# Optimization experiments

Measured on AMD Instinct MI355X. Metric: run time of the kernel, lower is better.

## Reference

```python
import jax, jax.numpy as jnp
import numpy as np

K_ATTRS = 16  # fixed number of attribute clusters (torch.unique made static for jit)
NEG_INF = jnp.float32(-1e9)


def setup_inputs() -> dict:
    key = jax.random.key(0)
    ks = jax.random.split(key, 20)
    B, T, V, D, H = 4096, 200, 100000, 64, 64
    M0, M1 = 256, 128
    FC_IN = D + D + H + D  # 256
    s = 0.02
    f32 = jnp.float32
    inp = {
        "item_id": jax.random.randint(ks[0], (B,), 0, V),
        "hist_item_ids": jax.random.randint(ks[1], (B, T), 0, V),
        "hist_item_attributes": jax.random.randint(ks[2], (B, T), 0, K_ATTRS),
        "emb_table": s * jax.random.normal(ks[3], (V, D), dtype=f32),
        "au_W1": s * jax.random.normal(ks[4], (4 * D, H), dtype=f32),
        "au_b1": jnp.zeros((H,), f32),
        "au_W2": s * jax.random.normal(ks[5], (H, 1), dtype=f32),
        "au_b2": jnp.zeros((1,), f32),
        "gru_Wx": s * jax.random.normal(ks[6], (D, 3 * H), dtype=f32),
        "gru_Wh": s * jax.random.normal(ks[7], (H, 3 * H), dtype=f32),
        "gru_b": jnp.zeros((3 * H,), f32),
        "fc_W0": s * jax.random.normal(ks[8], (FC_IN, M0), dtype=f32),
        "fc_b0": jnp.zeros((M0,), f32),
        "fc_W1": s * jax.random.normal(ks[9], (M0, M1), dtype=f32),
        "fc_b1": jnp.zeros((M1,), f32),
        "final_W": s * jax.random.normal(ks[10], (M1, 1), dtype=f32),
        "final_b": jnp.zeros((1,), f32),
    }
    return inp


def reference(item_id, hist_item_ids, hist_item_attributes, emb_table,
              au_W1, au_b1, au_W2, au_b2, gru_Wx, gru_Wh, gru_b,
              fc_W0, fc_b0, fc_W1, fc_b1, final_W, final_b):
    item = emb_table[item_id]            # [B,D]
    hist = emb_table[hist_item_ids]      # [B,T,D]
    B = item.shape[0]
    H = gru_Wh.shape[0]

    # --- DIEN: GRU over history, final hidden state ---
    xp = hist @ gru_Wx + gru_b           # [B,T,3H]

    def step(h, x):
        gz, gr, gn = jnp.split(h @ gru_Wh, 3, axis=-1)
        xz, xr, xn = jnp.split(x, 3, axis=-1)
        z = jax.nn.sigmoid(xz + gz)
        r = jax.nn.sigmoid(xr + gr)
        n = jnp.tanh(xn + r * gn)
        return (1.0 - z) * n + z * h, None

    h0 = jnp.zeros((B, H), hist.dtype)
    interest_evolution, _ = jax.lax.scan(step, h0, jnp.swapaxes(xp, 0, 1))  # [B,H]

    # --- DIN-style activation unit: score each key against the target item ---
    def act_unit(q, keys):  # q:[B,D], keys:[B,N,D] -> [B,N,1]
        qe = jnp.broadcast_to(q[:, None, :], keys.shape)
        feat = jnp.concatenate([keys, qe, keys - qe, keys * qe], axis=-1)
        hid = jax.nn.relu(feat @ au_W1 + au_b1)
        return hid @ au_W2 + au_b2

    w1 = act_unit(item, hist)                    # [B,T,1]
    user_interest_l1 = jnp.sum(w1 * hist, axis=1)  # [B,D]

    # --- attribute_group: per-attribute masked softmax + weighted sum ---
    mask = hist_item_attributes[..., None] == jnp.arange(K_ATTRS)  # [B,T,K]
    logits = jnp.where(mask, w1, NEG_INF)        # [B,T,K]
    probs = jax.nn.softmax(logits, axis=1) * mask
    cluster = jnp.einsum('btk,btd->bkd', probs, hist)  # [B,K,D]

    w2 = act_unit(item, cluster)                 # [B,K,1]
    user_interest_l2 = jnp.sum(w2 * cluster, axis=1)  # [B,D]

    combined = jnp.concatenate(
        [user_interest_l1, user_interest_l2, interest_evolution, item], axis=1)
    x = jax.nn.relu(combined @ fc_W0 + fc_b0)
    x = jax.nn.relu(x @ fc_W1 + fc_b1)
    out = x @ final_W + final_b                  # [B,1]
    return jax.nn.sigmoid(out[:, 0])             # [B]
```

## Files before the change

kernel.cpp:

```cpp
#include <hip/hip_runtime.h>
#include <hip/hip_bf16.h>

#define B_   4096
#define T_   200
#define KA   16

#define OFF_BG  0
#define OFF_QP  (OFF_BG  + B_*T_)
#define OFF_UI1 (OFF_QP  + B_*64)
#define OFF_UI2 (OFF_UI1 + B_*64)
#define OFF_HF  (OFF_UI2 + B_*64)
#define OFF_CL  (OFF_HF  + B_*64)

typedef __attribute__((ext_vector_type(8))) short bf16x8;
typedef __attribute__((ext_vector_type(4))) float f32x4;

__device__ __forceinline__ float sigmoidf_(float x) {
  return 1.f / (1.f + __expf(-x));
}
__device__ __forceinline__ float sigf(float x) {
  return __builtin_amdgcn_rcpf(1.f + __builtin_amdgcn_exp2f(-1.44269504f * x));
}
__device__ __forceinline__ float tanhfast(float y) {
  return 1.f - 2.f * __builtin_amdgcn_rcpf(1.f + __builtin_amdgcn_exp2f(2.88539008f * y));
}
__device__ __forceinline__ short f2bf(float x) {
  unsigned u = __float_as_uint(x);
  unsigned r = (u + 0x7fffu + ((u >> 16) & 1u)) >> 16;
  return (short)r;
}
__device__ __forceinline__ unsigned cvtpk(float lo, float hi) {
  unsigned r;
  asm("v_cvt_pk_bf16_f32 %0, %1, %2" : "=v"(r) : "v"(lo), "v"(hi));
  return r;
}
union BF8 { bf16x8 v; unsigned u[4]; };

__device__ __forceinline__ bf16x8 pack8(float4 f0, float4 f1) {
  BF8 a;
  a.u[0] = cvtpk(f0.x, f0.y);
  a.u[1] = cvtpk(f0.z, f0.w);
  a.u[2] = cvtpk(f1.x, f1.y);
  a.u[3] = cvtpk(f1.z, f1.w);
  return a.v;
}
__device__ __forceinline__ bf16x8 pack8m(float4 f0, float4 f1,
                                         float4 q0, float4 q1) {
  BF8 a;
  a.u[0] = cvtpk(f0.x*q0.x, f0.y*q0.y);
  a.u[1] = cvtpk(f0.z*q0.z, f0.w*q0.w);
  a.u[2] = cvtpk(f1.x*q1.x, f1.y*q1.y);
  a.u[3] = cvtpk(f1.z*q1.z, f1.w*q1.w);
  return a.v;
}


__global__ __launch_bounds__(256) void k_act1(
    const int* __restrict__ item_id, const int* __restrict__ hist_ids,
    const int* __restrict__ attrs,
    const float* __restrict__ emb, const float* __restrict__ auW1,
    const float* __restrict__ aub1, const float* __restrict__ auW2,
    const float* __restrict__ aub2,
    float* __restrict__ qp_out, float* __restrict__ ui1_out,
    float* __restrict__ cluster_out, short* __restrict__ bg_out)
{
  __shared__ short sB2[8192];
  __shared__ float sAcc[4][KA][64];
  __shared__ float sW1[208];
  __shared__ float sP[200];
  __shared__ float sM[KA], sE[KA];
  __shared__ float sItem[64], sQp[64];
  __shared__ float sQpP[4][64];
  __shared__ float sUi[4][64];
  __shared__ int   sIds[200], sAttr[200];

  const int b = blockIdx.x;
  const int tid = threadIdx.x;
  const int wave = tid >> 6, lane = tid & 63;
  const int g = lane >> 4;
  const int c15 = lane & 15;
  const int itrow = item_id[b];

  for (int idx = tid; idx < 8192; idx += 256) {
    const int k = idx >> 6, col = idx & 63;
    float v;
    if (k < 64) v = auW1[k*64 + col] + auW1[2*4096 + k*64 + col];
    else        v = auW1[3*4096 + (k-64)*64 + col];
    short bv = f2bf(v);
    int dst = ((k >> 5)*4 + ((k >> 3) & 3))*512 + col*8 + (k & 7);
    sB2[dst] = bv;
    if (b == 0) bg_out[dst] = bv;
  }
  if (tid < 64) sItem[tid] = emb[(size_t)itrow*64 + tid];
  if (tid < T_) {
    sIds[tid]  = hist_ids[(size_t)b*T_ + tid];
    sAttr[tid] = attrs[(size_t)b*T_ + tid];
  }
  for (int i = tid; i < 4*KA*64; i += 256) ((float*)sAcc)[i] = 0.f;
  __syncthreads();

  {
    const int j = tid & 63, iq = tid >> 6;
    float acc = 0.f;
    #pragma unroll
    for (int ii = 0; ii < 16; ++ii) {
      const int i = iq*16 + ii;
      acc += sItem[i] * (auW1[(64+i)*64 + j] - auW1[(128+i)*64 + j]);
    }
    sQpP[iq][j] = acc;
  }
  __syncthreads();
  if (tid < 64) {
    float q = aub1[tid] + sQpP[0][tid] + sQpP[1][tid] + sQpP[2][tid] + sQpP[3][tid];
    sQp[tid] = q;
    qp_out[(size_t)b*64 + tid] = q;
  }
  __syncthreads();

  const float4* itemp = (const float4*)(emb + (size_t)itrow*64);
  float4 q0 = itemp[g*2],     q1 = itemp[g*2 + 1];
  float4 q2 = itemp[8 + g*2], q3 = itemp[8 + g*2 + 1];

  bf16x8 bfr[4][4];
  #pragma unroll
  for (int kk = 0; kk < 4; ++kk) {
    #pragma unroll
    for (int n = 0; n < 4; ++n)
      bfr[kk][n] = *(const bf16x8*)&sB2[(kk*4 + g)*512 + (n*16 + c15)*8];
  }
  float w2v[4], qpv[4];
  #pragma unroll
  for (int n = 0; n < 4; ++n) {
    w2v[n] = auW2[n*16 + c15];
    qpv[n] = sQp[n*16 + c15];
  }
  const float b2v = aub2[0];

  for (int tt = wave; tt < 13; tt += 4) {
    const int t = tt*16 + c15;
    float4 k0{0,0,0,0}, k1{0,0,0,0}, k2{0,0,0,0}, k3{0,0,0,0};
    if (t < T_) {
      const float4* kp = (const float4*)(emb + (size_t)sIds[t]*64);
      k0 = kp[g*2];     k1 = kp[g*2 + 1];
      k2 = kp[8 + g*2]; k3 = kp[8 + g*2 + 1];
    }
    bf16x8 a0 = pack8(k0, k1);
    bf16x8 a1 = pack8(k2, k3);
    bf16x8 a2 = pack8m(k0, k1, q0, q1);
    bf16x8 a3 = pack8m(k2, k3, q2, q3);

    f32x4 acc[4];
    #pragma unroll
    for (int n = 0; n < 4; ++n) acc[n] = f32x4{qpv[n], qpv[n], qpv[n], qpv[n]};
    #pragma unroll
    for (int n = 0; n < 4; ++n) {
      acc[n] = __builtin_amdgcn_mfma_f32_16x16x32_bf16(a0, bfr[0][n], acc[n], 0, 0, 0);
      acc[n] = __builtin_amdgcn_mfma_f32_16x16x32_bf16(a1, bfr[1][n], acc[n], 0, 0, 0);
      acc[n] = __builtin_amdgcn_mfma_f32_16x16x32_bf16(a2, bfr[2][n], acc[n], 0, 0, 0);
      acc[n] = __builtin_amdgcn_mfma_f32_16x16x32_bf16(a3, bfr[3][n], acc[n], 0, 0, 0);
    }
    float ws[4] = {0.f, 0.f, 0.f, 0.f};
    #pragma unroll
    for (int n = 0; n < 4; ++n) {
      #pragma unroll
      for (int r = 0; r < 4; ++r)
        ws[r] += fmaxf(acc[n][r], 0.f) * w2v[n];
    }
    #pragma unroll
    for (int r = 0; r < 4; ++r) {
      ws[r] += __shfl_xor(ws[r], 1);
      ws[r] += __shfl_xor(ws[r], 2);
      ws[r] += __shfl_xor(ws[r], 4);
      ws[r] += __shfl_xor(ws[r], 8);
      ws[r] += b2v;
    }
    if (c15 == 0) {
      #pragma unroll
      for (int r = 0; r < 4; ++r) {
        const int trow = tt*16 + g*4 + r;
        if (trow < T_) sW1[trow] = ws[r];
      }
    }
  }
  __syncthreads();

  for (int k = wave; k < KA; k += 4) {
    float m = -1e9f;
    for (int tt4 = 0; tt4 < 4; ++tt4) {
      int t = tt4*64 + lane;
      if (t < T_ && sAttr[t] == k) m = fmaxf(m, sW1[t]);
    }
    #pragma unroll
    for (int off = 32; off > 0; off >>= 1) m = fmaxf(m, __shfl_xor(m, off));
    float e = 0.f;
    for (int tt4 = 0; tt4 < 4; ++tt4) {
      int t = tt4*64 + lane;
      if (t < T_ && sAttr[t] == k) e += __expf(sW1[t] - m);
    }
    #pragma unroll
    for (int off = 32; off > 0; off >>= 1) e += __shfl_xor(e, off);
    if (lane == 0) { sM[k] = m; sE[k] = e; }
  }
  __syncthreads();
  if (tid < T_) {
    int k = sAttr[tid];
    float e = sE[k];
    sP[tid] = (e > 0.f) ? __expf(sW1[tid] - sM[k]) * __builtin_amdgcn_rcpf(e) : 0.f;
  }
  __syncthreads();

  float uiacc = 0.f;
  for (int t = wave; t < T_; t += 4) {
    int k    = sAttr[t];
    float p  = sP[t];
    float wv = sW1[t];
    float v  = emb[(size_t)sIds[t]*64 + lane];
    sAcc[wave][k][lane] += p * v;
    uiacc += wv * v;
  }
  sUi[wave][lane] = uiacc;
  __syncthreads();

  for (int i = tid; i < KA*64; i += 256) {
    cluster_out[(size_t)b*(KA*64) + i] =
        sAcc[0][0][i] + sAcc[1][0][i] + sAcc[2][0][i] + sAcc[3][0][i];
  }
  if (tid < 64) {
    ui1_out[(size_t)b*64 + tid] =
        sUi[0][tid] + sUi[1][tid] + sUi[2][tid] + sUi[3][tid];
  }
}

#define GRU_ROWS 16
__global__ __launch_bounds__(512) void k_gru(
    const int* __restrict__ hist_ids, const float* __restrict__ emb,
    const float* __restrict__ Wx, const float* __restrict__ Wh,
    const float* __restrict__ gb, float* __restrict__ hfin_out)
{
  __shared__ short sH[2][16*64];
  __shared__ short sX[4][16*64];
  __shared__ int   sIds[16*200];

  const int tid  = threadIdx.x;
  const int w    = tid >> 6;
  const int lane = tid & 63;
  const int g    = lane >> 4;
  const int c15  = lane & 15;
  const int b0   = blockIdx.x * GRU_ROWS;

  for (int i = tid; i < 16*200; i += 512) {
    const int r = i / 200, t = i - r*200;
    sIds[i] = hist_ids[(size_t)(b0 + r)*T_ + t];
  }
  for (int i = tid; i < 16*64; i += 512) sH[0][i] = 0;
  __syncthreads();

  if (w >= 4) {
    const int stane = (w - 4)*64 + lane;
    const int srow  = stane >> 4;
    const int scol  = (stane & 15) * 4;
    const int sidx  = srow*64 + (((scol >> 3) ^ (srow & 7))*8) + (scol & 7);
    const int* idrow = &sIds[srow*200];
    #pragma unroll
    for (int p = 0; p < 2; ++p) {
      const float4 f = *(const float4*)(emb + (size_t)idrow[p]*64 + scol);
      uint2 u; u.x = cvtpk(f.x, f.y); u.y = cvtpk(f.z, f.w);
      *(uint2*)&sX[p][sidx] = u;
    }
    __syncthreads();
    for (int t = 0; t < T_; ++t) {
      const int t2 = (t + 2 < T_) ? (t + 2) : (T_ - 1);
      const float4 f = *(const float4*)(emb + (size_t)idrow[t2]*64 + scol);
      uint2 u; u.x = cvtpk(f.x, f.y); u.y = cvtpk(f.z, f.w);
      *(uint2*)&sX[(t + 2) & 3][sidx] = u;
      __syncthreads();
    }
  } else {
    bf16x8 bx[3][2], bh[3][2];
    #pragma unroll
    for (int l = 0; l < 3; ++l) {
      const int jb = (l*4 + w)*16 + c15;
      #pragma unroll
      for (int kk = 0; kk < 2; ++kk) {
        bf16x8 vx, vh;
        #pragma unroll
        for (int e = 0; e < 8; ++e) {
          const int krow = kk*32 + g*8 + e;
          vx[e] = f2bf(Wx[(size_t)krow*192 + jb]);
          vh[e] = f2bf(Wh[(size_t)krow*192 + jb]);
        }
        bx[l][kk] = vx; bh[l][kk] = vh;
      }
    }
    float bias[3];
    #pragma unroll
    for (int l = 0; l < 3; ++l) bias[l] = gb[l*64 + w*16 + c15];

    const int rs = c15 & 7;
    const int ridx0 = c15*64 + ((g    ) ^ rs)*8;
    const int ridx1 = c15*64 + ((g + 4) ^ rs)*8;
    int widx[4];
    {
      const int unit = w*2 + (c15 >> 3);
      #pragma unroll
      for (int r = 0; r < 4; ++r) {
        const int row = g*4 + r;
        widx[r] = row*64 + ((unit ^ (row & 7))*8) + (c15 & 7);
      }
    }
    float hold[4] = {0.f, 0.f, 0.f, 0.f};
    __syncthreads();

    #pragma unroll 2
    for (int t = 0; t < T_; ++t) {
      const short* hbuf = sH[t & 1];
      short*       hnxt = sH[(t & 1) ^ 1];
      const short* xbuf = sX[t & 3];

      bf16x8 ax0 = *(const bf16x8*)&xbuf[ridx0];
      bf16x8 ax1 = *(const bf16x8*)&xbuf[ridx1];
      bf16x8 ah0 = *(const bf16x8*)&hbuf[ridx0];
      bf16x8 ah1 = *(const bf16x8*)&hbuf[ridx1];

      f32x4 aX[3], aH[3];
      #pragma unroll
      for (int l = 0; l < 3; ++l) {
        aX[l] = f32x4{bias[l], bias[l], bias[l], bias[l]};
        aH[l] = f32x4{0.f, 0.f, 0.f, 0.f};
      }
      #pragma unroll
      for (int l = 0; l < 3; ++l) {
        aH[l] = __builtin_amdgcn_mfma_f32_16x16x32_bf16(ah0, bh[l][0], aH[l], 0, 0, 0);
        aH[l] = __builtin_amdgcn_mfma_f32_16x16x32_bf16(ah1, bh[l][1], aH[l], 0, 0, 0);
        aX[l] = __builtin_amdgcn_mfma_f32_16x16x32_bf16(ax0, bx[l][0], aX[l], 0, 0, 0);
        aX[l] = __builtin_amdgcn_mfma_f32_16x16x32_bf16(ax1, bx[l][1], aX[l], 0, 0, 0);
      }

      #pragma unroll
      for (int r = 0; r < 4; ++r) {
        float z  = sigf(aX[0][r] + aH[0][r]);
        float rr = sigf(aX[1][r] + aH[1][r]);
        float nn = tanhfast(aX[2][r] + rr * aH[2][r]);
        hold[r] = nn + z * (hold[r] - nn);
        hnxt[widx[r]] = f2bf(hold[r]);
      }
      __syncthreads();
    }

    #pragma unroll
    for (int r = 0; r < 4; ++r)
      hfin_out[(size_t)(b0 + g*4 + r)*64 + w*16 + c15] = hold[r];
  }
}

__global__ __launch_bounds__(256) void k_act2(
    const int* __restrict__ item_id, const float* __restrict__ emb,
    const float* __restrict__ auW2, const float* __restrict__ aub2,
    const float* __restrict__ qp_in, const float* __restrict__ cluster_in,
    const short* __restrict__ bg_in, float* __restrict__ ui2_out)
{
  __shared__ short sB2[8192];
  __shared__ float sWs[4][16];
  __shared__ float sWf[16];
  __shared__ float sUi[4][64];

  const int b = blockIdx.x;
  const int tid = threadIdx.x;
  const int wave = tid >> 6, lane = tid & 63;
  const int g = lane >> 4;
  const int c15 = lane & 15;
  const int itrow = item_id[b];

  for (int i = tid; i < 4096; i += 256)
    ((unsigned*)sB2)[i] = ((const unsigned*)bg_in)[i];
  __syncthreads();

  const float4* itemp = (const float4*)(emb + (size_t)itrow*64);
  float4 q0 = itemp[g*2],     q1 = itemp[g*2 + 1];
  float4 q2 = itemp[8 + g*2], q3 = itemp[8 + g*2 + 1];
  const float4* kp = (const float4*)(cluster_in + (size_t)b*(KA*64) + c15*64);
  float4 k0 = kp[g*2],     k1 = kp[g*2 + 1];
  float4 k2 = kp[8 + g*2], k3 = kp[8 + g*2 + 1];
  bf16x8 a0 = pack8(k0, k1);
  bf16x8 a1 = pack8(k2, k3);
  bf16x8 a2 = pack8m(k0, k1, q0, q1);
  bf16x8 a3 = pack8m(k2, k3, q2, q3);

  const float qpv = qp_in[(size_t)b*64 + wave*16 + c15];
  const float w2v = auW2[wave*16 + c15];
  f32x4 acc = f32x4{qpv, qpv, qpv, qpv};
  acc = __builtin_amdgcn_mfma_f32_16x16x32_bf16(a0, *(const bf16x8*)&sB2[(0*4+g)*512 + (wave*16+c15)*8], acc, 0, 0, 0);
  acc = __builtin_amdgcn_mfma_f32_16x16x32_bf16(a1, *(const bf16x8*)&sB2[(1*4+g)*512 + (wave*16+c15)*8], acc, 0, 0, 0);
  acc = __builtin_amdgcn_mfma_f32_16x16x32_bf16(a2, *(const bf16x8*)&sB2[(2*4+g)*512 + (wave*16+c15)*8], acc, 0, 0, 0);
  acc = __builtin_amdgcn_mfma_f32_16x16x32_bf16(a3, *(const bf16x8*)&sB2[(3*4+g)*512 + (wave*16+c15)*8], acc, 0, 0, 0);

  float ws[4];
  #pragma unroll
  for (int r = 0; r < 4; ++r) {
    float v = fmaxf(acc[r], 0.f) * w2v;
    v += __shfl_xor(v, 1);
    v += __shfl_xor(v, 2);
    v += __shfl_xor(v, 4);
    v += __shfl_xor(v, 8);
    ws[r] = v;
  }
  if (c15 == 0) {
    #pragma unroll
    for (int r = 0; r < 4; ++r) sWs[wave][g*4 + r] = ws[r];
  }
  __syncthreads();
  if (tid < KA)
    sWf[tid] = sWs[0][tid] + sWs[1][tid] + sWs[2][tid] + sWs[3][tid] + aub2[0];
  __syncthreads();

  float uiacc = 0.f;
  #pragma unroll
  for (int kk = 0; kk < 4; ++kk) {
    const int k = wave*4 + kk;
    uiacc += sWf[k] * cluster_in[(size_t)b*(KA*64) + k*64 + lane];
  }
  sUi[wave][lane] = uiacc;
  __syncthreads();
  if (tid < 64) {
    ui2_out[(size_t)b*64 + tid] =
        sUi[0][tid] + sUi[1][tid] + sUi[2][tid] + sUi[3][tid];
  }
}

#define MLP_ROWS 16
__global__ __launch_bounds__(256) void k_mlp(
    const int* __restrict__ item_id, const float* __restrict__ emb,
    const float* __restrict__ ui1, const float* __restrict__ ui2,
    const float* __restrict__ hfin,
    const float* __restrict__ W0, const float* __restrict__ b0,
    const float* __restrict__ W1, const float* __restrict__ b1,
    const float* __restrict__ fW, const float* __restrict__ fb,
    float* __restrict__ out)
{
  __shared__ float sC[MLP_ROWS][256];
  __shared__ float sX0[MLP_ROWS][256];
  __shared__ float sX1[MLP_ROWS][128];
  const int tid = threadIdx.x;
  const int rb  = blockIdx.x * MLP_ROWS;

  for (int idx = tid; idx < MLP_ROWS*256; idx += 256) {
    int r = idx >> 8, c = idx & 255;
    size_t row = (size_t)(rb + r);
    float v;
    if (c < 64)       v = ui1[row*64 + c];
    else if (c < 128) v = ui2[row*64 + (c-64)];
    else if (c < 192) v = hfin[row*64 + (c-128)];
    else              v = emb[(size_t)item_id[row]*64 + (c-192)];
    sC[r][c] = v;
  }
  __syncthreads();
  {
    float acc[MLP_ROWS];
    #pragma unroll
    for (int r = 0; r < MLP_ROWS; ++r) acc[r] = b0[tid];
    #pragma unroll 4
    for (int i = 0; i < 256; ++i) {
      float w = W0[(size_t)i*256 + tid];
      #pragma unroll
      for (int r = 0; r < MLP_ROWS; ++r) acc[r] += sC[r][i] * w;
    }
    #pragma unroll
    for (int r = 0; r < MLP_ROWS; ++r) sX0[r][tid] = fmaxf(acc[r], 0.f);
  }
  __syncthreads();
  if (tid < 128) {
    float acc[MLP_ROWS];
    #pragma unroll
    for (int r = 0; r < MLP_ROWS; ++r) acc[r] = b1[tid];
    #pragma unroll 4
    for (int i = 0; i < 256; ++i) {
      float w = W1[(size_t)i*128 + tid];
      #pragma unroll
      for (int r = 0; r < MLP_ROWS; ++r) acc[r] += sX0[r][i] * w;
    }
    #pragma unroll
    for (int r = 0; r < MLP_ROWS; ++r) sX1[r][tid] = fmaxf(acc[r], 0.f);
  }
  __syncthreads();
  {
    int r = tid >> 4, l16 = tid & 15;
    float p = 0.f;
    for (int i = l16; i < 128; i += 16) p += sX1[r][i] * fW[i];
    #pragma unroll
    for (int off = 8; off > 0; off >>= 1) p += __shfl_xor(p, off);
    if (l16 == 0) {
      float logit = p + fb[0];
      out[rb + r] = sigmoidf_(logit);
    }
  }
}

extern "C" void kernel_launch(void* const* d_in, const int* in_sizes, int n_in,
                              void* d_out, int out_size, void* d_ws, size_t ws_size,
                              hipStream_t stream)
{
  const int*   item_id  = (const int*)d_in[0];
  const int*   hist_ids = (const int*)d_in[1];
  const int*   attrs    = (const int*)d_in[2];
  const float* emb      = (const float*)d_in[3];
  const float* auW1     = (const float*)d_in[4];
  const float* aub1     = (const float*)d_in[5];
  const float* auW2     = (const float*)d_in[6];
  const float* aub2     = (const float*)d_in[7];
  const float* gWx      = (const float*)d_in[8];
  const float* gWh      = (const float*)d_in[9];
  const float* gb       = (const float*)d_in[10];
  const float* W0       = (const float*)d_in[11];
  const float* b0       = (const float*)d_in[12];
  const float* W1       = (const float*)d_in[13];
  const float* b1       = (const float*)d_in[14];
  const float* fW       = (const float*)d_in[15];
  const float* fb       = (const float*)d_in[16];

  float* out = (float*)d_out;
  float* ws  = (float*)d_ws;
  short* bg      = (short*)(ws + OFF_BG);
  float* qp      = ws + OFF_QP;
  float* ui1     = ws + OFF_UI1;
  float* ui2     = ws + OFF_UI2;
  float* hfin    = ws + OFF_HF;
  float* cluster = ws + OFF_CL;

  k_act1<<<B_, 256, 0, stream>>>(item_id, hist_ids, attrs, emb, auW1, aub1,
                                 auW2, aub2, qp, ui1, cluster, bg);
  k_gru<<<B_/GRU_ROWS, 512, 0, stream>>>(hist_ids, emb, gWx, gWh, gb, hfin);
  k_act2<<<B_, 256, 0, stream>>>(item_id, emb, auW2, aub2, qp, cluster, bg,
                                 ui2);
  k_mlp<<<B_/MLP_ROWS, 256, 0, stream>>>(item_id, emb, ui1, ui2, hfin,
                                         W0, b0, W1, b1, fW, fb, out);
}
```

Before: 361.6 us.

## Precompute bf16 activation-unit weights once in a prep kernel, alias LDS, prefetch gathers

```diff
diff --git a/kernel.cpp b/kernel.cpp
--- a/kernel.cpp
+++ b/kernel.cpp
@@ -6,6 +6,7 @@
 #define KA   16
 
 #define OFF_BG  0
+#define OFF_WQ  4096
 #define OFF_QP  (OFF_BG  + B_*T_)
 #define OFF_UI1 (OFF_QP  + B_*64)
 #define OFF_UI2 (OFF_UI1 + B_*64)
@@ -55,17 +56,34 @@
 }
 
 
+__global__ __launch_bounds__(256) void k_prep(
+    const float* __restrict__ auW1, short* __restrict__ bg,
+    float* __restrict__ wq)
+{
+  const int i = blockIdx.x*256 + threadIdx.x;
+  if (i < 8192) {
+    const int k = i >> 6, col = i & 63;
+    float v;
+    if (k < 64) v = auW1[k*64 + col] + auW1[2*4096 + k*64 + col];
+    else        v = auW1[3*4096 + (k-64)*64 + col];
+    bg[((k >> 5)*4 + ((k >> 3) & 3))*512 + col*8 + (k & 7)] = f2bf(v);
+  } else if (i < 12288) {
+    const int j = i - 8192;
+    wq[j] = auW1[(64 + (j >> 6))*64 + (j & 63)]
+          - auW1[(128 + (j >> 6))*64 + (j & 63)];
+  }
+}
+
 __global__ __launch_bounds__(256) void k_act1(
     const int* __restrict__ item_id, const int* __restrict__ hist_ids,
     const int* __restrict__ attrs,
-    const float* __restrict__ emb, const float* __restrict__ auW1,
-    const float* __restrict__ aub1, const float* __restrict__ auW2,
-    const float* __restrict__ aub2,
+    const float* __restrict__ emb, const float* __restrict__ aub1,
+    const float* __restrict__ auW2, const float* __restrict__ aub2,
+    const short* __restrict__ bg_in, const float* __restrict__ wq_in,
     float* __restrict__ qp_out, float* __restrict__ ui1_out,
-    float* __restrict__ cluster_out, short* __restrict__ bg_out)
+    float* __restrict__ cluster_out)
 {
-  __shared__ short sB2[8192];
-  __shared__ float sAcc[4][KA][64];
+  __shared__ __align__(16) char sPool[16384];
   __shared__ float sW1[208];
   __shared__ float sP[200];
   __shared__ float sM[KA], sE[KA];
@@ -74,6 +92,9 @@
   __shared__ float sUi[4][64];
   __shared__ int   sIds[200], sAttr[200];
 
+  short* sB2 = (short*)sPool;
+  float (*sAcc)[KA][64] = (float (*)[KA][64])sPool;
+
   const int b = blockIdx.x;
   const int tid = threadIdx.x;
   const int wave = tid >> 6, lane = tid & 63;
@@ -81,22 +102,13 @@
   const int c15 = lane & 15;
   const int itrow = item_id[b];
 
-  for (int idx = tid; idx < 8192; idx += 256) {
-    const int k = idx >> 6, col = idx & 63;
-    float v;
-    if (k < 64) v = auW1[k*64 + col] + auW1[2*4096 + k*64 + col];
-    else        v = auW1[3*4096 + (k-64)*64 + col];
-    short bv = f2bf(v);
-    int dst = ((k >> 5)*4 + ((k >> 3) & 3))*512 + col*8 + (k & 7);
-    sB2[dst] = bv;
-    if (b == 0) bg_out[dst] = bv;
-  }
+  for (int i = tid; i < 4096; i += 256)
+    ((unsigned*)sB2)[i] = ((const unsigned*)bg_in)[i];
   if (tid < 64) sItem[tid] = emb[(size_t)itrow*64 + tid];
   if (tid < T_) {
     sIds[tid]  = hist_ids[(size_t)b*T_ + tid];
     sAttr[tid] = attrs[(size_t)b*T_ + tid];
   }
-  for (int i = tid; i < 4*KA*64; i += 256) ((float*)sAcc)[i] = 0.f;
   __syncthreads();
 
   {
@@ -105,7 +117,7 @@
     #pragma unroll
     for (int ii = 0; ii < 16; ++ii) {
       const int i = iq*16 + ii;
-      acc += sItem[i] * (auW1[(64+i)*64 + j] - auW1[(128+i)*64 + j]);
+      acc += sItem[i] * wq_in[i*64 + j];
     }
     sQpP[iq][j] = acc;
   }
@@ -135,6 +147,9 @@
     qpv[n] = sQp[n*16 + c15];
   }
   const float b2v = aub2[0];
+  __syncthreads();
+
+  for (int i = tid; i < 4*KA*64; i += 256) ((float*)sAcc)[i] = 0.f;
 
   for (int tt = wave; tt < 13; tt += 4) {
     const int t = tt*16 + c15;
@@ -210,13 +225,17 @@
   __syncthreads();
 
   float uiacc = 0.f;
-  for (int t = wave; t < T_; t += 4) {
-    int k    = sAttr[t];
-    float p  = sP[t];
-    float wv = sW1[t];
-    float v  = emb[(size_t)sIds[t]*64 + lane];
-    sAcc[wave][k][lane] += p * v;
-    uiacc += wv * v;
+  {
+    float vcur = emb[(size_t)sIds[wave]*64 + lane];
+    for (int t = wave; t < T_; t += 4) {
+      const int tn = t + 4;
+      float vnext = 0.f;
+      if (tn < T_) vnext = emb[(size_t)sIds[tn]*64 + lane];
+      const int k = sAttr[t];
+      sAcc[wave][k][lane] += sP[t] * vcur;
+      uiacc += sW1[t] * vcur;
+      vcur = vnext;
+    }
   }
   sUi[wave][lane] = uiacc;
   __syncthreads();
@@ -520,14 +539,16 @@
   float* out = (float*)d_out;
   float* ws  = (float*)d_ws;
   short* bg      = (short*)(ws + OFF_BG);
+  float* wq      = ws + OFF_WQ;
   float* qp      = ws + OFF_QP;
   float* ui1     = ws + OFF_UI1;
   float* ui2     = ws + OFF_UI2;
   float* hfin    = ws + OFF_HF;
   float* cluster = ws + OFF_CL;
 
-  k_act1<<<B_, 256, 0, stream>>>(item_id, hist_ids, attrs, emb, auW1, aub1,
-                                 auW2, aub2, qp, ui1, cluster, bg);
+  k_prep<<<48, 256, 0, stream>>>(auW1, bg, wq);
+  k_act1<<<B_, 256, 0, stream>>>(item_id, hist_ids, attrs, emb, aub1,
+                                 auW2, aub2, bg, wq, qp, ui1, cluster);
   k_gru<<<B_/GRU_ROWS, 512, 0, stream>>>(hist_ids, emb, gWx, gWh, gb, hfin);
   k_act2<<<B_, 256, 0, stream>>>(item_id, emb, auW2, aub2, qp, cluster, bg,
                                  ui2);
```

After: 324.6 us. 10.3% less time.
